# Kernel optimization log

Measured on AMD Instinct MI355X. Metric: run time of the kernel, lower is better.

The kernel has to match this reference:

```python
import jax, jax.numpy as jnp
import numpy as np

BN_EPS = 1e-5

def setup_inputs() -> dict:
    key = jax.random.key(0)
    ks = jax.random.split(key, 4)
    B, S, H = 32, 4096, 768
    hidden_states = jax.random.normal(ks[0], (B, S, H), dtype=jnp.float32)
    attention_mask = jnp.ones((B, S), dtype=jnp.int32)
    boost = jax.random.randint(ks[1], (B, S), 0, 2, dtype=jnp.int32)
    attn_w = jax.random.normal(ks[2], (H,), dtype=jnp.float32) / np.sqrt(H)
    attn_b = jnp.zeros((), dtype=jnp.float32)
    fc_w = jax.random.normal(ks[3], (H, H), dtype=jnp.float32) / np.sqrt(H)
    fc_b = jnp.zeros((H,), dtype=jnp.float32)
    gamma = jnp.ones((H,), dtype=jnp.float32)
    beta = jnp.zeros((H,), dtype=jnp.float32)
    return {"hidden_states": hidden_states, "attention_mask": attention_mask,
            "boost": boost, "attn_w": attn_w, "attn_b": attn_b,
            "fc_w": fc_w, "fc_b": fc_b, "gamma": gamma, "beta": beta}


def reference(hidden_states, attention_mask, boost, attn_w, attn_b, fc_w, fc_b, gamma, beta):
    # scores: [B, S] = Linear(H -> 1) then squeeze
    scores = jnp.einsum('bsh,h->bs', hidden_states, attn_w) + attn_b
    # keyword boost: multiply by 3 where boost==1 (vectorized form of the token loop)
    mult = 1.0 + 2.0 * boost.astype(scores.dtype)
    scores = scores * mult
    # masked softmax over sequence dim
    scores = jnp.where(attention_mask == 0, -jnp.inf, scores)
    weights = jax.nn.softmax(scores, axis=1)  # [B, S]
    # weighted-sum pooling -> [B, H]
    context = jnp.einsum('bsh,bs->bh', hidden_states, weights)
    # BatchNorm1d (training mode: batch stats, biased variance)
    mean = jnp.mean(context, axis=0)
    var = jnp.mean(jnp.square(context - mean), axis=0)
    context = (context - mean) * jax.lax.rsqrt(var + BN_EPS) * gamma + beta
    # dropout is identity in eval mode
    # residual fc + ReLU
    out = jax.nn.relu(context @ fc_w.T + fc_b + context)
    return out
```

## Files before the change

### kernel.cpp

```cpp
#include <hip/hip_runtime.h>
#include <math.h>

constexpr int B = 32;
constexpr int S = 4096;
constexpr int H = 768;

constexpr int BLOCKS_PER_BATCH = 32;
constexpr int ROWS_PER_BLOCK   = S / BLOCKS_PER_BATCH;
constexpr int WAVES_PER_BLOCK  = 4;
constexpr int ROWS_PER_WAVE    = ROWS_PER_BLOCK / WAVES_PER_BLOCK;
constexpr int NPART            = B * BLOCKS_PER_BATCH;

__global__ __launch_bounds__(256)
void pool_partial(const float* __restrict__ hs,
                  const int*   __restrict__ mask,
                  const int*   __restrict__ boost,
                  const float* __restrict__ attn_w,
                  const float* __restrict__ attn_b,
                  float* __restrict__ pm, float* __restrict__ pl,
                  float* __restrict__ pc)
{
    const int blk  = blockIdx.x;
    const int b    = blk >> 5;
    const int kb   = blk & (BLOCKS_PER_BATCH - 1);
    const int tid  = threadIdx.x;
    const int w    = tid >> 6;
    const int lane = tid & 63;
    const int s0   = kb * ROWS_PER_BLOCK + w * ROWS_PER_WAVE;

    const float4 w0 = *reinterpret_cast<const float4*>(attn_w +       4 * lane);
    const float4 w1 = *reinterpret_cast<const float4*>(attn_w + 256 + 4 * lane);
    const float4 w2 = *reinterpret_cast<const float4*>(attn_w + 512 + 4 * lane);
    const float bias = attn_b[0];

    float m = -INFINITY, l = 0.0f;
    float c[12];
#pragma unroll
    for (int j = 0; j < 12; ++j) c[j] = 0.0f;

    const float* base = hs + (size_t)b * S * H;
    const int*   mrow = mask  + (size_t)b * S;
    const int*   brow = boost + (size_t)b * S;

    for (int r = 0; r < ROWS_PER_WAVE; ++r) {
        const int s = s0 + r;
        const float4* row = reinterpret_cast<const float4*>(base + (size_t)s * H);
        const float4 v0 = row[lane];
        const float4 v1 = row[64  + lane];
        const float4 v2 = row[128 + lane];

        float d = v0.x * w0.x + v0.y * w0.y + v0.z * w0.z + v0.w * w0.w
                + v1.x * w1.x + v1.y * w1.y + v1.z * w1.z + v1.w * w1.w
                + v2.x * w2.x + v2.y * w2.y + v2.z * w2.z + v2.w * w2.w;
#pragma unroll
        for (int off = 32; off > 0; off >>= 1) d += __shfl_xor(d, off, 64);

        const int   mk   = mrow[s];
        const float mult = 1.0f + 2.0f * (float)brow[s];
        const float score = (d + bias) * mult;

        if (mk != 0) {
            const float mn = fmaxf(m, score);
            const float sc = __expf(m - mn);
            const float p  = __expf(score - mn);
            l = l * sc + p;
            c[0]  = c[0]  * sc + p * v0.x;  c[1]  = c[1]  * sc + p * v0.y;
            c[2]  = c[2]  * sc + p * v0.z;  c[3]  = c[3]  * sc + p * v0.w;
            c[4]  = c[4]  * sc + p * v1.x;  c[5]  = c[5]  * sc + p * v1.y;
            c[6]  = c[6]  * sc + p * v1.z;  c[7]  = c[7]  * sc + p * v1.w;
            c[8]  = c[8]  * sc + p * v2.x;  c[9]  = c[9]  * sc + p * v2.y;
            c[10] = c[10] * sc + p * v2.z;  c[11] = c[11] * sc + p * v2.w;
            m = mn;
        }
    }

    __shared__ float sm[WAVES_PER_BLOCK], sl[WAVES_PER_BLOCK];
    __shared__ float scmb[WAVES_PER_BLOCK][H];
#pragma unroll
    for (int j = 0; j < 4; ++j) {
        scmb[w][4 * lane + j]       = c[j];
        scmb[w][256 + 4 * lane + j] = c[4 + j];
        scmb[w][512 + 4 * lane + j] = c[8 + j];
    }
    if (lane == 0) { sm[w] = m; sl[w] = l; }
    __syncthreads();

    const float M  = fmaxf(fmaxf(sm[0], sm[1]), fmaxf(sm[2], sm[3]));
    const float e0 = __expf(sm[0] - M), e1 = __expf(sm[1] - M);
    const float e2 = __expf(sm[2] - M), e3 = __expf(sm[3] - M);
    if (tid == 0) {
        pm[blk] = M;
        pl[blk] = sl[0] * e0 + sl[1] * e1 + sl[2] * e2 + sl[3] * e3;
    }
#pragma unroll
    for (int q = 0; q < 3; ++q) {
        const int h = tid + q * 256;
        pc[(size_t)blk * H + h] =
            scmb[0][h] * e0 + scmb[1][h] * e1 + scmb[2][h] * e2 + scmb[3][h] * e3;
    }
}

__global__ __launch_bounds__(256)
void pool_combine(const float* __restrict__ pm, const float* __restrict__ pl,
                  const float* __restrict__ pc, float* __restrict__ context)
{
    const int b   = blockIdx.x;
    const int tid = threadIdx.x;
    __shared__ float ss[BLOCKS_PER_BATCH];

    float M = -INFINITY;
    for (int i = 0; i < BLOCKS_PER_BATCH; ++i)
        M = fmaxf(M, pm[b * BLOCKS_PER_BATCH + i]);
    if (tid < BLOCKS_PER_BATCH)
        ss[tid] = __expf(pm[b * BLOCKS_PER_BATCH + tid] - M);
    __syncthreads();

    float L = 0.0f;
    for (int i = 0; i < BLOCKS_PER_BATCH; ++i)
        L += pl[b * BLOCKS_PER_BATCH + i] * ss[i];
    const float invL = 1.0f / L;

#pragma unroll
    for (int q = 0; q < 3; ++q) {
        const int h = tid + q * 256;
        float acc = 0.0f;
        for (int i = 0; i < BLOCKS_PER_BATCH; ++i)
            acc += pc[((size_t)b * BLOCKS_PER_BATCH + i) * H + h] * ss[i];
        context[b * H + h] = acc * invL;
    }
}

__global__ __launch_bounds__(256)
void batchnorm_k(const float* __restrict__ context,
                 const float* __restrict__ gamma, const float* __restrict__ beta,
                 float* __restrict__ chat)
{
    const int h = blockIdx.x * 256 + threadIdx.x;
    float x[B];
    float mean = 0.0f;
#pragma unroll
    for (int b = 0; b < B; ++b) { x[b] = context[b * H + h]; mean += x[b]; }
    mean *= (1.0f / B);
    float var = 0.0f;
#pragma unroll
    for (int b = 0; b < B; ++b) { const float d = x[b] - mean; var += d * d; }
    var *= (1.0f / B);
    const float inv = rsqrtf(var + 1e-5f);
    const float g = gamma[h], be = beta[h];
#pragma unroll
    for (int b = 0; b < B; ++b)
        chat[b * H + h] = (x[b] - mean) * inv * g + be;
}

__global__ __launch_bounds__(256)
void fc_relu_k(const float* __restrict__ chat, const float* __restrict__ fcw,
               const float* __restrict__ fcb, float* __restrict__ out)
{
    const int i = blockIdx.x * 256 + threadIdx.x;
    const int b = blockIdx.y;
    const float* cb = chat + (size_t)b * H;
    const float4* wr  = reinterpret_cast<const float4*>(fcw + (size_t)i * H);
    const float4* cbv = reinterpret_cast<const float4*>(cb);

    float acc = fcb[i];
#pragma unroll 4
    for (int hq = 0; hq < H / 4; ++hq) {
        const float4 wv = wr[hq];
        const float4 cv = cbv[hq];
        acc += wv.x * cv.x + wv.y * cv.y + wv.z * cv.z + wv.w * cv.w;
    }
    acc += cb[i];
    out[(size_t)b * H + i] = fmaxf(acc, 0.0f);
}

extern "C" void kernel_launch(void* const* d_in, const int* in_sizes, int n_in,
                              void* d_out, int out_size, void* d_ws, size_t ws_size,
                              hipStream_t stream)
{
    const float* hs     = (const float*)d_in[0];
    const int*   mask   = (const int*)d_in[1];
    const int*   boost  = (const int*)d_in[2];
    const float* attn_w = (const float*)d_in[3];
    const float* attn_b = (const float*)d_in[4];
    const float* fc_w   = (const float*)d_in[5];
    const float* fc_b   = (const float*)d_in[6];
    const float* gamma  = (const float*)d_in[7];
    const float* beta   = (const float*)d_in[8];
    float* out = (float*)d_out;

    float* ws      = (float*)d_ws;
    float* pm      = ws;
    float* pl      = pm + NPART;
    float* pc      = pl + NPART;
    float* context = pc + (size_t)NPART * H;
    float* chat    = context + B * H;

    pool_partial<<<dim3(NPART), 256, 0, stream>>>(hs, mask, boost, attn_w, attn_b,
                                                  pm, pl, pc);
    pool_combine<<<dim3(B), 256, 0, stream>>>(pm, pl, pc, context);
    batchnorm_k<<<dim3(H / 256), 256, 0, stream>>>(context, gamma, beta, chat);
    fc_relu_k<<<dim3(H / 256, B), 256, 0, stream>>>(chat, fc_w, fc_b, out);
}
```

Baseline: 115.0 us.

## Process two rows per wave with register prefetch and branchy online softmax

The pooling kernel now splits each wave into two 32-lane halves that each handle a different row, and software-prefetches the next row pair into registers while the current one is computed. Mask and boost values are loaded once per wave and broadcast with shuffles instead of being read per row. The online-softmax update skips rescaling when the max does not change. The combine kernel is spread over more blocks (a grid over H chunks and batches) with a wave-level reduction for the max and the sum. The cost is more register pressure from the prefetch buffers, plus an extra cross-half merge step.

After: 115.4 us. No clear change (+0.3%).

```diff
diff --git a/kernel.cpp b/kernel.cpp
--- a/kernel.cpp
+++ b/kernel.cpp
@@ -5,13 +5,12 @@
 constexpr int S = 4096;
 constexpr int H = 768;
 
-constexpr int BLOCKS_PER_BATCH = 32;
-constexpr int ROWS_PER_BLOCK   = S / BLOCKS_PER_BATCH;
-constexpr int WAVES_PER_BLOCK  = 4;
-constexpr int ROWS_PER_WAVE    = ROWS_PER_BLOCK / WAVES_PER_BLOCK;
-constexpr int NPART            = B * BLOCKS_PER_BATCH;
-
-__global__ __launch_bounds__(256)
+constexpr int BPB            = 32;
+constexpr int ROWS_PER_BLOCK = S / BPB;
+constexpr int ROWS_PER_WAVE  = ROWS_PER_BLOCK / 4;
+constexpr int NPART          = B * BPB;
+
+__global__ __launch_bounds__(256, 4)
 void pool_partial(const float* __restrict__ hs,
                   const int*   __restrict__ mask,
                   const int*   __restrict__ boost,
@@ -22,72 +21,123 @@
 {
     const int blk  = blockIdx.x;
     const int b    = blk >> 5;
-    const int kb   = blk & (BLOCKS_PER_BATCH - 1);
+    const int kb   = blk & (BPB - 1);
     const int tid  = threadIdx.x;
     const int w    = tid >> 6;
     const int lane = tid & 63;
-    const int s0   = kb * ROWS_PER_BLOCK + w * ROWS_PER_WAVE;
-
-    const float4 w0 = *reinterpret_cast<const float4*>(attn_w +       4 * lane);
-    const float4 w1 = *reinterpret_cast<const float4*>(attn_w + 256 + 4 * lane);
-    const float4 w2 = *reinterpret_cast<const float4*>(attn_w + 512 + 4 * lane);
+    const int g    = lane >> 5;
+    const int k    = lane & 31;
+
+    float4 wv[6];
+#pragma unroll
+    for (int j = 0; j < 6; ++j)
+        wv[j] = *reinterpret_cast<const float4*>(attn_w + 128 * j + 4 * k);
     const float bias = attn_b[0];
 
+    const int s0 = kb * ROWS_PER_BLOCK + w * ROWS_PER_WAVE;
+    const float* base = hs + (size_t)b * S * H;
+
+    {
+    }
+    const int   srl   = s0 + (lane & 31);
+    const int   mk0   = mask[(size_t)b * S + srl];
+    const float mult0 = mk0 ? (1.0f + 2.0f * (float)boost[(size_t)b * S + srl]) : 0.0f;
+
     float m = -INFINITY, l = 0.0f;
-    float c[12];
-#pragma unroll
-    for (int j = 0; j < 12; ++j) c[j] = 0.0f;
-
-    const float* base = hs + (size_t)b * S * H;
-    const int*   mrow = mask  + (size_t)b * S;
-    const int*   brow = boost + (size_t)b * S;
-
-    for (int r = 0; r < ROWS_PER_WAVE; ++r) {
-        const int s = s0 + r;
-        const float4* row = reinterpret_cast<const float4*>(base + (size_t)s * H);
-        const float4 v0 = row[lane];
-        const float4 v1 = row[64  + lane];
-        const float4 v2 = row[128 + lane];
-
-        float d = v0.x * w0.x + v0.y * w0.y + v0.z * w0.z + v0.w * w0.w
-                + v1.x * w1.x + v1.y * w1.y + v1.z * w1.z + v1.w * w1.w
-                + v2.x * w2.x + v2.y * w2.y + v2.z * w2.z + v2.w * w2.w;
-#pragma unroll
-        for (int off = 32; off > 0; off >>= 1) d += __shfl_xor(d, off, 64);
-
-        const int   mk   = mrow[s];
-        const float mult = 1.0f + 2.0f * (float)brow[s];
+    float4 c[6];
+#pragma unroll
+    for (int j = 0; j < 6; ++j) c[j] = make_float4(0.f, 0.f, 0.f, 0.f);
+
+    const float* rp = base + (size_t)(s0 + g) * H + 4 * k;
+    float4 v[6];
+#pragma unroll
+    for (int j = 0; j < 6; ++j)
+        v[j] = *reinterpret_cast<const float4*>(rp + 128 * j);
+
+    for (int i = 0; i < ROWS_PER_WAVE / 2; ++i) {
+        float4 vn[6];
+        const float* rn = rp + 2 * H;
+        if (i + 1 < ROWS_PER_WAVE / 2) {
+#pragma unroll
+            for (int j = 0; j < 6; ++j)
+                vn[j] = *reinterpret_cast<const float4*>(rn + 128 * j);
+        }
+
+        float d0 = 0.f, d1 = 0.f, d2 = 0.f, d3 = 0.f;
+#pragma unroll
+        for (int j = 0; j < 6; ++j) {
+            d0 = fmaf(v[j].x, wv[j].x, d0);
+            d1 = fmaf(v[j].y, wv[j].y, d1);
+            d2 = fmaf(v[j].z, wv[j].z, d2);
+            d3 = fmaf(v[j].w, wv[j].w, d3);
+        }
+        float d = (d0 + d1) + (d2 + d3);
+
+#pragma unroll
+        for (int off = 16; off >= 1; off >>= 1)
+            d += __shfl_xor(d, off, 64);
+
+        const float mult  = __shfl(mult0, 2 * i + g, 64);
         const float score = (d + bias) * mult;
 
-        if (mk != 0) {
-            const float mn = fmaxf(m, score);
-            const float sc = __expf(m - mn);
-            const float p  = __expf(score - mn);
-            l = l * sc + p;
-            c[0]  = c[0]  * sc + p * v0.x;  c[1]  = c[1]  * sc + p * v0.y;
-            c[2]  = c[2]  * sc + p * v0.z;  c[3]  = c[3]  * sc + p * v0.w;
-            c[4]  = c[4]  * sc + p * v1.x;  c[5]  = c[5]  * sc + p * v1.y;
-            c[6]  = c[6]  * sc + p * v1.z;  c[7]  = c[7]  * sc + p * v1.w;
-            c[8]  = c[8]  * sc + p * v2.x;  c[9]  = c[9]  * sc + p * v2.y;
-            c[10] = c[10] * sc + p * v2.z;  c[11] = c[11] * sc + p * v2.w;
-            m = mn;
+        if (mult > 0.0f) {
+            if (score <= m) {
+                const float p = __expf(score - m);
+                l += p;
+#pragma unroll
+                for (int j = 0; j < 6; ++j) {
+                    c[j].x = fmaf(p, v[j].x, c[j].x);
+                    c[j].y = fmaf(p, v[j].y, c[j].y);
+                    c[j].z = fmaf(p, v[j].z, c[j].z);
+                    c[j].w = fmaf(p, v[j].w, c[j].w);
+                }
+            } else {
+                const float sc = __expf(m - score);
+                m = score;
+                l = fmaf(l, sc, 1.0f);
+#pragma unroll
+                for (int j = 0; j < 6; ++j) {
+                    c[j].x = fmaf(c[j].x, sc, v[j].x);
+                    c[j].y = fmaf(c[j].y, sc, v[j].y);
+                    c[j].z = fmaf(c[j].z, sc, v[j].z);
+                    c[j].w = fmaf(c[j].w, sc, v[j].w);
+                }
+            }
         }
-    }
-
-    __shared__ float sm[WAVES_PER_BLOCK], sl[WAVES_PER_BLOCK];
-    __shared__ float scmb[WAVES_PER_BLOCK][H];
-#pragma unroll
-    for (int j = 0; j < 4; ++j) {
-        scmb[w][4 * lane + j]       = c[j];
-        scmb[w][256 + 4 * lane + j] = c[4 + j];
-        scmb[w][512 + 4 * lane + j] = c[8 + j];
-    }
-    if (lane == 0) { sm[w] = m; sl[w] = l; }
+#pragma unroll
+        for (int j = 0; j < 6; ++j) v[j] = vn[j];
+        rp = rn;
+    }
+
+    const float mo = __shfl_xor(m, 32, 64);
+    const float M2 = fmaxf(m, mo);
+    const float e  = (l > 0.0f) ? __expf(m - M2) : 0.0f;
+    float l2 = l * e;
+    l2 += __shfl_xor(l2, 32, 64);
+#pragma unroll
+    for (int j = 0; j < 6; ++j) {
+        c[j].x *= e; c[j].y *= e; c[j].z *= e; c[j].w *= e;
+        c[j].x += __shfl_xor(c[j].x, 32, 64);
+        c[j].y += __shfl_xor(c[j].y, 32, 64);
+        c[j].z += __shfl_xor(c[j].z, 32, 64);
+        c[j].w += __shfl_xor(c[j].w, 32, 64);
+    }
+
+    __shared__ float sm[4], sl[4];
+    __shared__ float scmb[4][H];
+    if (g == 0) {
+        if (k == 0) { sm[w] = M2; sl[w] = l2; }
+#pragma unroll
+        for (int j = 0; j < 6; ++j)
+            *reinterpret_cast<float4*>(&scmb[w][128 * j + 4 * k]) = c[j];
+    }
     __syncthreads();
 
     const float M  = fmaxf(fmaxf(sm[0], sm[1]), fmaxf(sm[2], sm[3]));
-    const float e0 = __expf(sm[0] - M), e1 = __expf(sm[1] - M);
-    const float e2 = __expf(sm[2] - M), e3 = __expf(sm[3] - M);
+    const float e0 = (sl[0] > 0.f) ? __expf(sm[0] - M) : 0.f;
+    const float e1 = (sl[1] > 0.f) ? __expf(sm[1] - M) : 0.f;
+    const float e2 = (sl[2] > 0.f) ? __expf(sm[2] - M) : 0.f;
+    const float e3 = (sl[3] > 0.f) ? __expf(sm[3] - M) : 0.f;
     if (tid == 0) {
         pm[blk] = M;
         pl[blk] = sl[0] * e0 + sl[1] * e1 + sl[2] * e2 + sl[3] * e3;
@@ -104,30 +154,34 @@
 void pool_combine(const float* __restrict__ pm, const float* __restrict__ pl,
                   const float* __restrict__ pc, float* __restrict__ context)
 {
-    const int b   = blockIdx.x;
+    const int qc  = blockIdx.x;
+    const int b   = blockIdx.y;
     const int tid = threadIdx.x;
-    __shared__ float ss[BLOCKS_PER_BATCH];
-
-    float M = -INFINITY;
-    for (int i = 0; i < BLOCKS_PER_BATCH; ++i)
-        M = fmaxf(M, pm[b * BLOCKS_PER_BATCH + i]);
-    if (tid < BLOCKS_PER_BATCH)
-        ss[tid] = __expf(pm[b * BLOCKS_PER_BATCH + tid] - M);
+    __shared__ float ss[BPB];
+    __shared__ float sinv;
+
+    if (tid < BPB) {
+        const float mv = pm[b * BPB + tid];
+        float M = mv;
+#pragma unroll
+        for (int off = 16; off >= 1; off >>= 1)
+            M = fmaxf(M, __shfl_xor(M, off, 64));
+        const float e = __expf(mv - M);
+        ss[tid] = e;
+        float lv = pl[b * BPB + tid] * e;
+#pragma unroll
+        for (int off = 16; off >= 1; off >>= 1)
+            lv += __shfl_xor(lv, off, 64);
+        if (tid == 0) sinv = 1.0f / lv;
+    }
     __syncthreads();
 
-    float L = 0.0f;
-    for (int i = 0; i < BLOCKS_PER_BATCH; ++i)
-        L += pl[b * BLOCKS_PER_BATCH + i] * ss[i];
-    const float invL = 1.0f / L;
-
-#pragma unroll
-    for (int q = 0; q < 3; ++q) {
-        const int h = tid + q * 256;
-        float acc = 0.0f;
-        for (int i = 0; i < BLOCKS_PER_BATCH; ++i)
-            acc += pc[((size_t)b * BLOCKS_PER_BATCH + i) * H + h] * ss[i];
-        context[b * H + h] = acc * invL;
-    }
+    const int h = qc * 256 + tid;
+    float acc = 0.0f;
+#pragma unroll 4
+    for (int i = 0; i < BPB; ++i)
+        acc = fmaf(pc[((size_t)b * BPB + i) * H + h], ss[i], acc);
+    context[b * H + h] = acc * sinv;
 }
 
 __global__ __launch_bounds__(256)
@@ -146,10 +200,10 @@
     for (int b = 0; b < B; ++b) { const float d = x[b] - mean; var += d * d; }
     var *= (1.0f / B);
     const float inv = rsqrtf(var + 1e-5f);
-    const float g = gamma[h], be = beta[h];
+    const float gq = gamma[h], be = beta[h];
 #pragma unroll
     for (int b = 0; b < B; ++b)
-        chat[b * H + h] = (x[b] - mean) * inv * g + be;
+        chat[b * H + h] = (x[b] - mean) * inv * gq + be;
 }
 
 __global__ __launch_bounds__(256)
@@ -165,9 +219,9 @@
     float acc = fcb[i];
 #pragma unroll 4
     for (int hq = 0; hq < H / 4; ++hq) {
-        const float4 wv = wr[hq];
-        const float4 cv = cbv[hq];
-        acc += wv.x * cv.x + wv.y * cv.y + wv.z * cv.z + wv.w * cv.w;
+        const float4 wvv = wr[hq];
+        const float4 cv  = cbv[hq];
+        acc += wvv.x * cv.x + wvv.y * cv.y + wvv.z * cv.z + wvv.w * cv.w;
     }
     acc += cb[i];
     out[(size_t)b * H + i] = fmaxf(acc, 0.0f);
@@ -197,7 +251,7 @@
 
     pool_partial<<<dim3(NPART), 256, 0, stream>>>(hs, mask, boost, attn_w, attn_b,
                                                   pm, pl, pc);
-    pool_combine<<<dim3(B), 256, 0, stream>>>(pm, pl, pc, context);
+    pool_combine<<<dim3(H / 256, B), 256, 0, stream>>>(pm, pl, pc, context);
     batchnorm_k<<<dim3(H / 256), 256, 0, stream>>>(context, gamma, beta, chat);
     fc_relu_k<<<dim3(H / 256, B), 256, 0, stream>>>(chat, fc_w, fc_b, out);
 }
```
